# Kernel tuning notes

Hardware: AMD Instinct MI355X
Metric: run time of the kernel (lower is better)

The kernel has to match this reference:

```python
import jax, jax.numpy as jnp
import numpy as np

H = 64  # hidden size
T_ENC = 20
T_DEC = 30


def setup_inputs() -> dict:
    key = jax.random.key(0)
    ks = jax.random.split(key, 12)
    B = 65536
    s = 0.1
    return {
        "input_traj": jax.random.normal(ks[0], (B, T_ENC, 2), jnp.float32),
        "W_ih_enc": jax.random.normal(ks[1], (4 * H, 2), jnp.float32) * s,
        "W_hh_enc": jax.random.normal(ks[2], (4 * H, H), jnp.float32) * s,
        "b_ih_enc": jax.random.normal(ks[3], (4 * H,), jnp.float32) * s,
        "b_hh_enc": jax.random.normal(ks[4], (4 * H,), jnp.float32) * s,
        "W_ih_dec": jax.random.normal(ks[5], (4 * H, H), jnp.float32) * s,
        "W_hh_dec": jax.random.normal(ks[6], (4 * H, H), jnp.float32) * s,
        "b_ih_dec": jax.random.normal(ks[7], (4 * H,), jnp.float32) * s,
        "b_hh_dec": jax.random.normal(ks[8], (4 * H,), jnp.float32) * s,
        "W_emb": jax.random.normal(ks[9], (2, H), jnp.float32) * s,
        "b_emb": jax.random.normal(ks[10], (2,), jnp.float32) * s,
    }


def _lstm_cell(x, h, c, Wih, Whh, bih, bhh):
    # PyTorch LSTMCell gate order: i, f, g, o
    gates = x @ Wih.T + bih + h @ Whh.T + bhh  # [B, 4H]
    i, f, g, o = jnp.split(gates, 4, axis=-1)
    i = jax.nn.sigmoid(i)
    f = jax.nn.sigmoid(f)
    g = jnp.tanh(g)
    o = jax.nn.sigmoid(o)
    c_new = f * c + i * g
    h_new = o * jnp.tanh(c_new)
    return h_new, c_new


def reference(input_traj, W_ih_enc, W_hh_enc, b_ih_enc, b_hh_enc,
              W_ih_dec, W_hh_dec, b_ih_dec, b_hh_dec, W_emb, b_emb):
    B = input_traj.shape[0]
    h0 = jnp.zeros((B, H), input_traj.dtype)
    c0 = jnp.zeros((B, H), input_traj.dtype)

    # Encoder: scan over 20 timesteps (time-major inputs)
    xs = jnp.transpose(input_traj, (1, 0, 2))  # [T_ENC, B, 2]

    def enc_step(carry, x_t):
        h, c = carry
        h, c = _lstm_cell(x_t, h, c, W_ih_enc, W_hh_enc, b_ih_enc, b_hh_enc)
        return (h, c), None

    (h, c), _ = jax.lax.scan(enc_step, (h0, c0), xs)

    # Decoder: 30 steps, input at each step is the current hidden state
    def dec_step(carry, _):
        h, c = carry
        h, c = _lstm_cell(h, h, c, W_ih_dec, W_hh_dec, b_ih_dec, b_hh_dec)
        pos = h @ W_emb.T + b_emb  # [B, 2]
        return (h, c), pos

    (_, _), pos_seq = jax.lax.scan(dec_step, (h, c), None, length=T_DEC)
    pred_traj = jnp.transpose(pos_seq, (1, 0, 2))  # [B, T_DEC, 2]
    return pred_traj
```

## Files before the change

kernel.cpp:

```cpp
#include <hip/hip_runtime.h>

#define T_ENC 20
#define T_DEC 30
#define WAVES 4
#define EPB (WAVES * 32)

typedef __attribute__((ext_vector_type(8))) _Float16 half8;
typedef __attribute__((ext_vector_type(16))) float f32x16;

#if __has_builtin(__builtin_amdgcn_exp2f)
#define EXP2F(x) __builtin_amdgcn_exp2f(x)
#else
#define EXP2F(x) exp2f(x)
#endif
#if __has_builtin(__builtin_amdgcn_rcpf)
#define RCPF(x) __builtin_amdgcn_rcpf(x)
#else
#define RCPF(x) (1.0f / (x))
#endif

#define LOG2E 1.4426950408889634f
#define TWO_LOG2E 2.8853900817779268f

#define MFMA16(a, b, c) __builtin_amdgcn_mfma_f32_32x32x16_f16(a, b, c, 0, 0, 0)

__device__ __forceinline__ unsigned short h2u(_Float16 h) {
  union { _Float16 h; unsigned short u; } v;
  v.h = h;
  return v.u;
}

__global__ __launch_bounds__(256, 1)
void SinglePrediction_88493506167138_kernel(
    const float* __restrict__ x,
    const float* __restrict__ W_ih_enc,
    const float* __restrict__ W_hh_enc,
    const float* __restrict__ b_ih_enc,
    const float* __restrict__ b_hh_enc,
    const float* __restrict__ W_ih_dec,
    const float* __restrict__ W_hh_dec,
    const float* __restrict__ b_ih_dec,
    const float* __restrict__ b_hh_dec,
    const float* __restrict__ W_emb,
    const float* __restrict__ b_emb,
    float* __restrict__ out,
    float* __restrict__ ws,
    int Btot, int use_ws)
{
  __shared__ __align__(16) unsigned short Wf[288 * 64];
  __shared__ __align__(16) unsigned short hTh[WAVES][32 * 64];
  __shared__ __align__(16) unsigned short hTl[WAVES][32 * 64];
  __shared__ float bsum_l[256];

  const int tid = threadIdx.x;
  const int lane = tid & 63;
  const int wid = tid >> 6;
  const int hi5 = lane >> 5;
  const int l31 = lane & 31;
  const int beb = blockIdx.x * EPB;

  for (int i = tid; i < 256 * 64; i += 256) {
    int row = i >> 6, k = i & 63;
    float sc = ((row >> 6) == 2) ? TWO_LOG2E : LOG2E;
    _Float16 wv = (_Float16)(W_hh_enc[i] * sc);
    Wf[(row << 6) | (k ^ ((row & 7) << 3))] = h2u(wv);
  }
  if (tid < 256) {
    float sc = ((tid >> 6) == 2) ? TWO_LOG2E : LOG2E;
    bsum_l[tid] = (b_ih_enc[tid] + b_hh_enc[tid]) * sc;
  }
  {
    float4 z = {0.f, 0.f, 0.f, 0.f};
    float4* p0 = (float4*)&hTh[wid][0];
    float4* p1 = (float4*)&hTl[wid][0];
    for (int i = lane; i < 256; i += 64) { p0[i] = z; p1[i] = z; }
  }
  __syncthreads();

  float biasv[8], wi0[8], wi1[8];
#pragma unroll
  for (int nt = 0; nt < 8; nt++) {
    int n = nt * 32 + l31;
    float sc = ((n >> 6) == 2) ? TWO_LOG2E : LOG2E;
    biasv[nt] = bsum_l[n];
    float2 wv = *(const float2*)&W_ih_enc[2 * n];
    wi0[nt] = wv.x * sc;
    wi1[nt] = wv.y * sc;
  }

  float c01[2][16];
#pragma unroll
  for (int p = 0; p < 2; p++)
#pragma unroll
    for (int q = 0; q < 16; q++) c01[p][q] = 0.f;

  const int sw = (l31 & 7) << 3;
  const int kbase = hi5 << 3;

  half8 ah[4], al[4];
  auto loadA = [&]() {
#pragma unroll
    for (int kt = 0; kt < 4; kt++) {
      int sk = (kt * 16 + kbase) ^ sw;
      ah[kt] = *(const half8*)&hTh[wid][(l31 << 6) + sk];
      al[kt] = *(const half8*)&hTl[wid][(l31 << 6) + sk];
    }
  };

  auto gemm_main = [&](f32x16 (&acc)[8]) {
#pragma unroll
    for (int kt = 0; kt < 4; kt++) {
      const int sk = (kt * 16 + kbase) ^ sw;
      half8 b[8];
#pragma unroll
      for (int nt = 0; nt < 8; nt++)
        b[nt] = *(const half8*)&Wf[((nt * 32 + l31) << 6) + sk];
#pragma unroll
      for (int nt = 0; nt < 8; nt++) acc[nt] = MFMA16(ah[kt], b[nt], acc[nt]);
#pragma unroll
      for (int nt = 0; nt < 8; nt++) acc[nt] = MFMA16(al[kt], b[nt], acc[nt]);
    }
  };

  auto finish_step = [&](f32x16 (&acc)[8]) {
#pragma unroll
    for (int p = 0; p < 2; p++)
#pragma unroll
      for (int q = 0; q < 16; q++) {
        float ig = RCPF(1.f + EXP2F(-acc[0 + p][q]));
        float fg = RCPF(1.f + EXP2F(-acc[2 + p][q]));
        float eg = EXP2F(acc[4 + p][q]);
        float gg = 1.f - 2.f * RCPF(eg + 1.f);
        float og = RCPF(1.f + EXP2F(-acc[6 + p][q]));
        float cn = fmaf(fg, c01[p][q], ig * gg);
        c01[p][q] = cn;
        float ec = EXP2F(TWO_LOG2E * cn);
        float th = 1.f - 2.f * RCPF(ec + 1.f);
        float hn = og * th;
        _Float16 hh = (_Float16)hn;
        _Float16 hl = (_Float16)(hn - (float)hh);
        const int row = (q & 3) + 8 * (q >> 2) + 4 * hi5;
        const int col = l31 + 32 * p;
        const int si = (row << 6) | (col ^ ((row & 7) << 3));
        hTh[wid][si] = h2u(hh);
        hTl[wid][si] = h2u(hl);
      }
  };

#pragma unroll 1
  for (int t = 0; t < T_ENC; t++) {
    loadA();
    f32x16 acc[8];
#pragma unroll
    for (int q = 0; q < 16; q++) {
      const int row = (q & 3) + 8 * (q >> 2) + 4 * hi5;
      const float2 xq =
          *(const float2*)&x[((size_t)(beb + wid * 32 + row)) * 40 + 2 * t];
#pragma unroll
      for (int nt = 0; nt < 8; nt++)
        acc[nt][q] = fmaf(xq.x, wi0[nt], fmaf(xq.y, wi1[nt], biasv[nt]));
    }
    gemm_main(acc);
    finish_step(acc);
  }

  __syncthreads();
  for (int i = tid; i < 288 * 64; i += 256) {
    int row = i >> 6, k = i & 63;
    float w;
    if (row < 256) {
      float sc = ((row >> 6) == 2) ? TWO_LOG2E : LOG2E;
      w = (W_ih_dec[i] + W_hh_dec[i]) * sc;
    } else if (row < 258) {
      w = W_emb[(row - 256) * 64 + k];
    } else {
      w = 0.f;
    }
    _Float16 wv = (_Float16)w;
    Wf[(row << 6) | (k ^ ((row & 7) << 3))] = h2u(wv);
  }
  if (tid < 256) {
    float sc = ((tid >> 6) == 2) ? TWO_LOG2E : LOG2E;
    bsum_l[tid] = (b_ih_dec[tid] + b_hh_dec[tid]) * sc;
  }
  __syncthreads();

#pragma unroll
  for (int nt = 0; nt < 8; nt++) biasv[nt] = bsum_l[nt * 32 + l31];
  const float bev = (l31 == 0) ? b_emb[0] : b_emb[1];

  auto do_pos = [&](int tout) {
    f32x16 accP;
#pragma unroll
    for (int q = 0; q < 16; q++) accP[q] = 0.f;
#pragma unroll
    for (int kt = 0; kt < 4; kt++) {
      int sk = (kt * 16 + kbase) ^ sw;
      int r = 256 + l31;
      half8 be = *(const half8*)&Wf[(r << 6) + sk];
      accP = MFMA16(ah[kt], be, accP);
      accP = MFMA16(al[kt], be, accP);
    }
    if (l31 < 2) {
#pragma unroll
      for (int q = 0; q < 16; q++) {
        int row = (q & 3) + 8 * (q >> 2) + 4 * hi5;
        size_t e = (size_t)(beb + wid * 32 + row);
        float v = accP[q] + bev;
        if (use_ws) {
          ws[((size_t)tout * Btot + e) * 2 + l31] = v;
        } else {
          out[e * 60 + 2 * tout + l31] = v;
        }
      }
    }
  };

#pragma unroll 1
  for (int t = 0; t < T_DEC; t++) {
    loadA();
    if (t > 0) do_pos(t - 1);
    f32x16 acc[8];
#pragma unroll
    for (int nt = 0; nt < 8; nt++)
#pragma unroll
      for (int q = 0; q < 16; q++) acc[nt][q] = biasv[nt];
    gemm_main(acc);
    finish_step(acc);
  }
  loadA();
  do_pos(T_DEC - 1);
}

__global__ __launch_bounds__(256)
void pos_transpose_kernel(const float* __restrict__ ws,
                          float* __restrict__ out, int Btot) {
  const int e = blockIdx.x * 256 + threadIdx.x;
  float2 v[T_DEC];
#pragma unroll
  for (int t = 0; t < T_DEC; t++)
    v[t] = ((const float2*)ws)[(size_t)t * Btot + e];
  float2* o = (float2*)(out + (size_t)e * 60);
#pragma unroll
  for (int t = 0; t < T_DEC; t++) o[t] = v[t];
}

extern "C" void kernel_launch(void* const* d_in, const int* in_sizes, int n_in,
                              void* d_out, int out_size, void* d_ws, size_t ws_size,
                              hipStream_t stream) {
  const float* x        = (const float*)d_in[0];
  const float* W_ih_enc = (const float*)d_in[1];
  const float* W_hh_enc = (const float*)d_in[2];
  const float* b_ih_enc = (const float*)d_in[3];
  const float* b_hh_enc = (const float*)d_in[4];
  const float* W_ih_dec = (const float*)d_in[5];
  const float* W_hh_dec = (const float*)d_in[6];
  const float* b_ih_dec = (const float*)d_in[7];
  const float* b_hh_dec = (const float*)d_in[8];
  const float* W_emb    = (const float*)d_in[9];
  const float* b_emb    = (const float*)d_in[10];
  float* out = (float*)d_out;

  const int B = in_sizes[0] / (T_ENC * 2);
  const int grid = B / EPB;
  const size_t ws_needed = (size_t)B * T_DEC * 2 * sizeof(float);
  const int use_ws = (ws_size >= ws_needed) ? 1 : 0;

  hipLaunchKernelGGL(SinglePrediction_88493506167138_kernel,
                     dim3(grid), dim3(256), 0, stream,
                     x, W_ih_enc, W_hh_enc, b_ih_enc, b_hh_enc,
                     W_ih_dec, W_hh_dec, b_ih_dec, b_hh_dec,
                     W_emb, b_emb, out, (float*)d_ws, B, use_ws);
  if (use_ws) {
    hipLaunchKernelGGL(pos_transpose_kernel, dim3(B / 256), dim3(256), 0,
                       stream, (const float*)d_ws, out, B);
  }
}
```

Measured before the change: 629.4 us.

## Process two 32-row batch tiles per wave and fold encoder input projection into MFMA

Each wave now handles 64 batch elements as two independent 32-row tiles, sharing each LDS-loaded weight fragment across both tiles' MFMAs and interleaving two independent accumulator chains. The encoder input projection, previously done with per-element FMAs and 16 scattered global loads per step, becomes one extra MFMA per tile using a padded fp16 hi/lo-split input and a small LDS weight table. This halves the grid, so fewer blocks run per CU. Register pressure roughly doubles (two sets of 8 f32x16 accumulators plus A fragments), which risks spills or lower overlap.

Result: slower. 798.3 us (+26.8%).

```diff
diff --git a/kernel.cpp b/kernel.cpp
--- a/kernel.cpp
+++ b/kernel.cpp
@@ -3,7 +3,8 @@
 #define T_ENC 20
 #define T_DEC 30
 #define WAVES 4
-#define EPB (WAVES * 32)
+#define EPW 64
+#define EPB (WAVES * EPW)
 
 typedef __attribute__((ext_vector_type(8))) _Float16 half8;
 typedef __attribute__((ext_vector_type(16))) float f32x16;
@@ -48,8 +49,9 @@
     int Btot, int use_ws)
 {
   __shared__ __align__(16) unsigned short Wf[288 * 64];
-  __shared__ __align__(16) unsigned short hTh[WAVES][32 * 64];
-  __shared__ __align__(16) unsigned short hTl[WAVES][32 * 64];
+  __shared__ __align__(16) unsigned short Wx[256 * 16];
+  __shared__ __align__(16) unsigned short hTh[WAVES][2][32 * 64];
+  __shared__ __align__(16) unsigned short hTl[WAVES][2][32 * 64];
   __shared__ float bsum_l[256];
 
   const int tid = threadIdx.x;
@@ -62,8 +64,13 @@
   for (int i = tid; i < 256 * 64; i += 256) {
     int row = i >> 6, k = i & 63;
     float sc = ((row >> 6) == 2) ? TWO_LOG2E : LOG2E;
-    _Float16 wv = (_Float16)(W_hh_enc[i] * sc);
-    Wf[(row << 6) | (k ^ ((row & 7) << 3))] = h2u(wv);
+    Wf[(row << 6) | (k ^ ((row & 7) << 3))] = h2u((_Float16)(W_hh_enc[i] * sc));
+  }
+  for (int i = tid; i < 256 * 16; i += 256) {
+    int r = i >> 4, k = i & 15;
+    float sc = ((r >> 6) == 2) ? TWO_LOG2E : LOG2E;
+    float v = (k < 4) ? W_ih_enc[2 * r + (k & 1)] * sc : 0.f;
+    Wx[i] = h2u((_Float16)v);
   }
   if (tid < 256) {
     float sc = ((tid >> 6) == 2) ? TWO_LOG2E : LOG2E;
@@ -71,58 +78,53 @@
   }
   {
     float4 z = {0.f, 0.f, 0.f, 0.f};
-    float4* p0 = (float4*)&hTh[wid][0];
-    float4* p1 = (float4*)&hTl[wid][0];
-    for (int i = lane; i < 256; i += 64) { p0[i] = z; p1[i] = z; }
+    float4* p0 = (float4*)&hTh[wid][0][0];
+    float4* p1 = (float4*)&hTl[wid][0][0];
+    for (int i = lane; i < 512; i += 64) { p0[i] = z; p1[i] = z; }
   }
   __syncthreads();
 
-  float biasv[8], wi0[8], wi1[8];
-#pragma unroll
-  for (int nt = 0; nt < 8; nt++) {
-    int n = nt * 32 + l31;
-    float sc = ((n >> 6) == 2) ? TWO_LOG2E : LOG2E;
-    biasv[nt] = bsum_l[n];
-    float2 wv = *(const float2*)&W_ih_enc[2 * n];
-    wi0[nt] = wv.x * sc;
-    wi1[nt] = wv.y * sc;
-  }
-
-  float c01[2][16];
+  float biasv[8];
+#pragma unroll
+  for (int nt = 0; nt < 8; nt++) biasv[nt] = bsum_l[nt * 32 + l31];
+
+  float cA[2][16], cB[2][16];
 #pragma unroll
   for (int p = 0; p < 2; p++)
 #pragma unroll
-    for (int q = 0; q < 16; q++) c01[p][q] = 0.f;
+    for (int q = 0; q < 16; q++) { cA[p][q] = 0.f; cB[p][q] = 0.f; }
 
   const int sw = (l31 & 7) << 3;
   const int kbase = hi5 << 3;
 
-  half8 ah[4], al[4];
+  half8 ahA[4], alA[4], ahB[4], alB[4];
   auto loadA = [&]() {
 #pragma unroll
     for (int kt = 0; kt < 4; kt++) {
       int sk = (kt * 16 + kbase) ^ sw;
-      ah[kt] = *(const half8*)&hTh[wid][(l31 << 6) + sk];
-      al[kt] = *(const half8*)&hTl[wid][(l31 << 6) + sk];
-    }
-  };
-
-  auto gemm_main = [&](f32x16 (&acc)[8]) {
+      ahA[kt] = *(const half8*)&hTh[wid][0][(l31 << 6) + sk];
+      alA[kt] = *(const half8*)&hTl[wid][0][(l31 << 6) + sk];
+      ahB[kt] = *(const half8*)&hTh[wid][1][(l31 << 6) + sk];
+      alB[kt] = *(const half8*)&hTl[wid][1][(l31 << 6) + sk];
+    }
+  };
+
+  auto gemm_main = [&](f32x16 (&aA)[8], f32x16 (&aB)[8]) {
 #pragma unroll
     for (int kt = 0; kt < 4; kt++) {
       const int sk = (kt * 16 + kbase) ^ sw;
-      half8 b[8];
-#pragma unroll
-      for (int nt = 0; nt < 8; nt++)
-        b[nt] = *(const half8*)&Wf[((nt * 32 + l31) << 6) + sk];
-#pragma unroll
-      for (int nt = 0; nt < 8; nt++) acc[nt] = MFMA16(ah[kt], b[nt], acc[nt]);
-#pragma unroll
-      for (int nt = 0; nt < 8; nt++) acc[nt] = MFMA16(al[kt], b[nt], acc[nt]);
-    }
-  };
-
-  auto finish_step = [&](f32x16 (&acc)[8]) {
+#pragma unroll
+      for (int nt = 0; nt < 8; nt++) {
+        const half8 b = *(const half8*)&Wf[((nt * 32 + l31) << 6) + sk];
+        aA[nt] = MFMA16(ahA[kt], b, aA[nt]);
+        aB[nt] = MFMA16(ahB[kt], b, aB[nt]);
+        aA[nt] = MFMA16(alA[kt], b, aA[nt]);
+        aB[nt] = MFMA16(alB[kt], b, aB[nt]);
+      }
+    }
+  };
+
+  auto finish = [&](f32x16 (&acc)[8], float (&c)[2][16], int g) {
 #pragma unroll
     for (int p = 0; p < 2; p++)
 #pragma unroll
@@ -132,8 +134,8 @@
         float eg = EXP2F(acc[4 + p][q]);
         float gg = 1.f - 2.f * RCPF(eg + 1.f);
         float og = RCPF(1.f + EXP2F(-acc[6 + p][q]));
-        float cn = fmaf(fg, c01[p][q], ig * gg);
-        c01[p][q] = cn;
+        float cn = fmaf(fg, c[p][q], ig * gg);
+        c[p][q] = cn;
         float ec = EXP2F(TWO_LOG2E * cn);
         float th = 1.f - 2.f * RCPF(ec + 1.f);
         float hn = og * th;
@@ -142,26 +144,41 @@
         const int row = (q & 3) + 8 * (q >> 2) + 4 * hi5;
         const int col = l31 + 32 * p;
         const int si = (row << 6) | (col ^ ((row & 7) << 3));
-        hTh[wid][si] = h2u(hh);
-        hTl[wid][si] = h2u(hl);
+        hTh[wid][g][si] = h2u(hh);
+        hTl[wid][g][si] = h2u(hl);
       }
   };
 
 #pragma unroll 1
   for (int t = 0; t < T_ENC; t++) {
     loadA();
-    f32x16 acc[8];
-#pragma unroll
-    for (int q = 0; q < 16; q++) {
-      const int row = (q & 3) + 8 * (q >> 2) + 4 * hi5;
-      const float2 xq =
-          *(const float2*)&x[((size_t)(beb + wid * 32 + row)) * 40 + 2 * t];
-#pragma unroll
-      for (int nt = 0; nt < 8; nt++)
-        acc[nt][q] = fmaf(xq.x, wi0[nt], fmaf(xq.y, wi1[nt], biasv[nt]));
-    }
-    gemm_main(acc);
-    finish_step(acc);
+    f32x16 accA[8], accB[8];
+#pragma unroll
+    for (int nt = 0; nt < 8; nt++)
+#pragma unroll
+      for (int q = 0; q < 16; q++) { accA[nt][q] = biasv[nt]; accB[nt][q] = biasv[nt]; }
+    const float m = (hi5 == 0) ? 1.f : 0.f;
+    const float2 xA =
+        *(const float2*)&x[((size_t)(beb + wid * EPW + l31)) * 40 + 2 * t];
+    const float2 xB =
+        *(const float2*)&x[((size_t)(beb + wid * EPW + 32 + l31)) * 40 + 2 * t];
+    const float xA0 = xA.x * m, xA1 = xA.y * m;
+    const float xB0 = xB.x * m, xB1 = xB.y * m;
+    _Float16 a0h = (_Float16)xA0, a1h = (_Float16)xA1;
+    _Float16 a0l = (_Float16)(xA0 - (float)a0h), a1l = (_Float16)(xA1 - (float)a1h);
+    _Float16 b0h = (_Float16)xB0, b1h = (_Float16)xB1;
+    _Float16 b0l = (_Float16)(xB0 - (float)b0h), b1l = (_Float16)(xB1 - (float)b1h);
+    const half8 a5A = {a0h, a1h, a0l, a1l, (_Float16)0.f, (_Float16)0.f, (_Float16)0.f, (_Float16)0.f};
+    const half8 a5B = {b0h, b1h, b0l, b1l, (_Float16)0.f, (_Float16)0.f, (_Float16)0.f, (_Float16)0.f};
+#pragma unroll
+    for (int nt = 0; nt < 8; nt++) {
+      const half8 bx = *(const half8*)&Wx[((nt * 32 + l31) << 4) + kbase];
+      accA[nt] = MFMA16(a5A, bx, accA[nt]);
+      accB[nt] = MFMA16(a5B, bx, accB[nt]);
+    }
+    gemm_main(accA, accB);
+    finish(accA, cA, 0);
+    finish(accB, cB, 1);
   }
 
   __syncthreads();
@@ -176,8 +193,7 @@
     } else {
       w = 0.f;
     }
-    _Float16 wv = (_Float16)w;
-    Wf[(row << 6) | (k ^ ((row & 7) << 3))] = h2u(wv);
+    Wf[(row << 6) | (k ^ ((row & 7) << 3))] = h2u((_Float16)w);
   }
   if (tid < 256) {
     float sc = ((tid >> 6) == 2) ? TWO_LOG2E : LOG2E;
@@ -189,7 +205,7 @@
   for (int nt = 0; nt < 8; nt++) biasv[nt] = bsum_l[nt * 32 + l31];
   const float bev = (l31 == 0) ? b_emb[0] : b_emb[1];
 
-  auto do_pos = [&](int tout) {
+  auto do_pos = [&](half8 (&ah)[4], half8 (&al)[4], int gofs, int tout) {
     f32x16 accP;
 #pragma unroll
     for (int q = 0; q < 16; q++) accP[q] = 0.f;
@@ -205,7 +221,7 @@
 #pragma unroll
       for (int q = 0; q < 16; q++) {
         int row = (q & 3) + 8 * (q >> 2) + 4 * hi5;
-        size_t e = (size_t)(beb + wid * 32 + row);
+        size_t e = (size_t)(beb + wid * EPW + gofs + row);
         float v = accP[q] + bev;
         if (use_ws) {
           ws[((size_t)tout * Btot + e) * 2 + l31] = v;
@@ -219,17 +235,22 @@
 #pragma unroll 1
   for (int t = 0; t < T_DEC; t++) {
     loadA();
-    if (t > 0) do_pos(t - 1);
-    f32x16 acc[8];
+    if (t > 0) {
+      do_pos(ahA, alA, 0, t - 1);
+      do_pos(ahB, alB, 32, t - 1);
+    }
+    f32x16 accA[8], accB[8];
 #pragma unroll
     for (int nt = 0; nt < 8; nt++)
 #pragma unroll
-      for (int q = 0; q < 16; q++) acc[nt][q] = biasv[nt];
-    gemm_main(acc);
-    finish_step(acc);
+      for (int q = 0; q < 16; q++) { accA[nt][q] = biasv[nt]; accB[nt][q] = biasv[nt]; }
+    gemm_main(accA, accB);
+    finish(accA, cA, 0);
+    finish(accB, cB, 1);
   }
   loadA();
-  do_pos(T_DEC - 1);
+  do_pos(ahA, alA, 0, T_DEC - 1);
+  do_pos(ahB, alB, 32, T_DEC - 1);
 }
 
 __global__ __launch_bounds__(256)
```
